# Kernel tuning notes

Hardware: AMD Instinct MI355X
Metric: run time of the kernel (lower is better)

The kernel has to match this reference:

```python
import jax, jax.numpy as jnp
import numpy as np

B, C, H, W = 64, 256, 56, 56
SCALES = (1, 2, 4, 8)  # scale[:groups] with groups=4; sum = 15 pooled maps


def setup_inputs() -> dict:
    key = jax.random.key(0)
    k1, k2 = jax.random.split(key)
    x = jax.random.normal(k1, (B, C, H, W), dtype=jnp.float32)
    # weight: [num_fea=H*W, sum(scales)=15]; small init (original fills 0, which
    # would make the gate identically sigmoid(0)=0.5 — use small random instead)
    weight = jax.random.normal(k2, (H * W, 15), dtype=jnp.float32) * 0.02
    return {"x": x, "weight": weight}


def reference(x, weight):
    b, c, h, w = x.shape
    hw = h * w
    # Multi-scale channel-group mean pooling: for scale i, split channels into
    # i equal groups (c divisible by all scales) and mean over each group.
    # Equivalent to the original's loop of c*j//i : c*(j+1)//i slices.
    feats = [x.reshape(b, i, c // i, hw).mean(axis=2) for i in SCALES]
    t = jnp.concatenate(feats, axis=1)  # [b, 15, hw]
    # Points(): normalize across the 15 pooled features per spatial location
    mean = t.mean(axis=1, keepdims=True)           # [b, 1, hw]
    std = t.std(axis=1, keepdims=True)             # unbiased=False (ddof=0)
    tn = (t - mean) / std                          # [b, 15, hw]
    # _style_integration: per-pixel weighted sum over the 15 features
    z = jnp.einsum('bfs,sf->bs', tn, weight)       # [b, hw]
    gate = jax.nn.sigmoid(z).reshape(b, 1, h, w)
    return x * gate
```

## Files before the change

kernel.cpp:

```cpp
#include <hip/hip_runtime.h>
#include <math.h>


constexpr int C_   = 256;
constexpr int HW_  = 3136;
constexpr int B_   = 64;
constexpr int SPW_ = 16;
constexpr int TPI_ = HW_ / SPW_;
constexpr int WPB_ = 4;

__device__ __forceinline__ float4 shx4(float4 a, int m) {
  float4 r;
  r.x = __shfl_xor(a.x, m);
  r.y = __shfl_xor(a.y, m);
  r.z = __shfl_xor(a.z, m);
  r.w = __shfl_xor(a.w, m);
  return r;
}
__device__ __forceinline__ float4 add4(float4 a, float4 b) {
  float4 r; r.x = a.x + b.x; r.y = a.y + b.y; r.z = a.z + b.z; r.w = a.w + b.w;
  return r;
}

__global__ __launch_bounds__(256, 4) void ppca_fused(
    const float* __restrict__ x, const float* __restrict__ wgt,
    float* __restrict__ out)
{
  const int lane = threadIdx.x & 63;
  const int wav  = threadIdx.x >> 6;
  const unsigned W   = blockIdx.x * WPB_ + wav;
  const unsigned b   = W / TPI_;
  const unsigned til = W - b * TPI_;
  const int sp0 = til * SPW_;

  const int s4 = lane & 3;
  const int c0 = lane >> 2;

  const size_t off = (size_t)b * C_ * HW_ + (size_t)c0 * 16 * HW_
                   + (size_t)sp0 + (size_t)(s4 << 2);
  const float* xb = x + off;
  float* ob = out + off;

  float4 v[16];
  #pragma unroll
  for (int i = 0; i < 16; ++i)
    v[i] = *(const float4*)(xb + (size_t)i * HW_);

  float4 ps = v[0];
  #pragma unroll
  for (int i = 1; i < 16; ++i) ps = add4(ps, v[i]);

  const float4 t1 = add4(ps, shx4(ps, 4));
  const float4 t2 = add4(t1, shx4(t1, 8));
  const float4 t3 = add4(t2, shx4(t2, 16));
  const float4 t4 = add4(t3, shx4(t3, 32));

  float4 m4;
  m4.x = t4.x * (1.f / 256.f); m4.y = t4.y * (1.f / 256.f);
  m4.z = t4.z * (1.f / 256.f); m4.w = t4.w * (1.f / 256.f);

  const float* wr = wgt + (size_t)sp0 * 15;
  const int i128 = 1 + (c0 >> 3);
  const int i64  = 3 + (c0 >> 2);
  const int i32  = 7 + (c0 >> 1);

  float4 zn, sq;
#define DO_SPATIAL(J, T1c, T2c, T3c, Mc, ZNc, SQc)                           \
  {                                                                          \
    const float* wp = wr + ((s4 << 2) + J) * 15;                             \
    const float w128 = wp[i128];                                             \
    const float w64  = wp[i64];                                              \
    const float w32  = wp[i32];                                              \
    const float u1 = T1c * (1.f / 32.f)  - Mc;                               \
    const float u2 = T2c * (1.f / 64.f)  - Mc;                               \
    const float u3 = T3c * (1.f / 128.f) - Mc;                               \
    ZNc = u1 * w32 * 0.5f + u2 * w64 * 0.25f + u3 * w128 * 0.125f;           \
    SQc = u1 * u1 * 0.5f  + u2 * u2 * 0.25f  + u3 * u3 * 0.125f;             \
  }
  DO_SPATIAL(0, t1.x, t2.x, t3.x, m4.x, zn.x, sq.x)
  DO_SPATIAL(1, t1.y, t2.y, t3.y, m4.y, zn.y, sq.y)
  DO_SPATIAL(2, t1.z, t2.z, t3.z, m4.z, zn.z, sq.z)
  DO_SPATIAL(3, t1.w, t2.w, t3.w, m4.w, zn.w, sq.w)
#undef DO_SPATIAL

  #pragma unroll
  for (int d = 4; d <= 32; d <<= 1) {
    zn = add4(zn, shx4(zn, d));
    sq = add4(sq, shx4(sq, d));
  }

  float4 g;
#define GATE(ZNc, SQc, Gc)                                                   \
  {                                                                          \
    const float var = SQc * (1.f / 15.f);                                    \
    const float inv = 1.f / sqrtf(var);                                      \
    const float z   = ZNc * inv;                                             \
    Gc = 1.f / (1.f + __expf(-z));                                           \
  }
  GATE(zn.x, sq.x, g.x)
  GATE(zn.y, sq.y, g.y)
  GATE(zn.z, sq.z, g.z)
  GATE(zn.w, sq.w, g.w)
#undef GATE

  #pragma unroll
  for (int i = 0; i < 16; ++i) {
    float4 vv = v[i];
    vv.x *= g.x; vv.y *= g.y; vv.z *= g.z; vv.w *= g.w;
    *(float4*)(ob + (size_t)i * HW_) = vv;
  }
}

extern "C" void kernel_launch(void* const* d_in, const int* in_sizes, int n_in,
                              void* d_out, int out_size, void* d_ws, size_t ws_size,
                              hipStream_t stream) {
  const float* x = (const float*)d_in[0];
  const float* w = (const float*)d_in[1];
  float* out = (float*)d_out;
  (void)in_sizes; (void)n_in; (void)out_size; (void)d_ws; (void)ws_size;

  dim3 grid(B_ * TPI_ / WPB_);
  dim3 block(256);
  ppca_fused<<<grid, block, 0, stream>>>(x, w, out);
}
```

Before: 343.0 us.

## Process multiple spatial tiles per wave with double-buffered register prefetch

Each wave now handles 8 consecutive tiles of 8 spatial positions instead of one tile of 16. The next tile's loads are issued into a second register buffer before the current tile is reduced and stored, so memory latency overlaps with compute. Lane mapping changes to 32 channel groups by 2 spatial quads, with one more shuffle reduction stage. The grid shrinks by a factor of K, and two 8-element float4 buffers raise register pressure, which may limit occupancy.

```diff
diff --git a/kernel.cpp b/kernel.cpp
--- a/kernel.cpp
+++ b/kernel.cpp
@@ -5,9 +5,12 @@
 constexpr int C_   = 256;
 constexpr int HW_  = 3136;
 constexpr int B_   = 64;
-constexpr int SPW_ = 16;
+constexpr int SPW_ = 8;
 constexpr int TPI_ = HW_ / SPW_;
+constexpr int NT_  = B_ * TPI_;
+constexpr int K_   = 8;
 constexpr int WPB_ = 4;
+constexpr int GRID_ = NT_ / (K_ * WPB_);
 
 __device__ __forceinline__ float4 shx4(float4 a, int m) {
   float4 r;
@@ -22,60 +25,59 @@
   return r;
 }
 
-__global__ __launch_bounds__(256, 4) void ppca_fused(
-    const float* __restrict__ x, const float* __restrict__ wgt,
-    float* __restrict__ out)
-{
-  const int lane = threadIdx.x & 63;
-  const int wav  = threadIdx.x >> 6;
-  const unsigned W   = blockIdx.x * WPB_ + wav;
-  const unsigned b   = W / TPI_;
-  const unsigned til = W - b * TPI_;
-  const int sp0 = til * SPW_;
+__device__ __forceinline__ const float* tbase(const float* x, unsigned t,
+                                              int c0, int s4) {
+  const unsigned b   = t / TPI_;
+  const unsigned til = t - b * TPI_;
+  return x + (size_t)b * C_ * HW_ + (size_t)c0 * 8 * HW_
+           + (size_t)(til * SPW_) + (size_t)(s4 << 2);
+}
 
-  const int s4 = lane & 3;
-  const int c0 = lane >> 2;
+__device__ __forceinline__ void tload(float4 v[8], const float* x, unsigned t,
+                                      int c0, int s4) {
+  const float* p = tbase(x, t, c0, s4);
+  #pragma unroll
+  for (int i = 0; i < 8; ++i)
+    v[i] = *(const float4*)(p + (size_t)i * HW_);
+}
 
-  const size_t off = (size_t)b * C_ * HW_ + (size_t)c0 * 16 * HW_
-                   + (size_t)sp0 + (size_t)(s4 << 2);
-  const float* xb = x + off;
-  float* ob = out + off;
-
-  float4 v[16];
-  #pragma unroll
-  for (int i = 0; i < 16; ++i)
-    v[i] = *(const float4*)(xb + (size_t)i * HW_);
-
+__device__ __forceinline__ void tcs(float4 v[8], const float* __restrict__ x,
+                                    const float* __restrict__ wgt,
+                                    float* __restrict__ out, unsigned t,
+                                    int c0, int s4) {
   float4 ps = v[0];
   #pragma unroll
-  for (int i = 1; i < 16; ++i) ps = add4(ps, v[i]);
-
-  const float4 t1 = add4(ps, shx4(ps, 4));
-  const float4 t2 = add4(t1, shx4(t1, 8));
-  const float4 t3 = add4(t2, shx4(t2, 16));
-  const float4 t4 = add4(t3, shx4(t3, 32));
+  for (int i = 1; i < 8; ++i) ps = add4(ps, v[i]);
+  const float4 p16 = add4(ps,  shx4(ps, 2));
+  const float4 t1  = add4(p16, shx4(p16, 4));
+  const float4 t2  = add4(t1,  shx4(t1, 8));
+  const float4 t3  = add4(t2,  shx4(t2, 16));
+  const float4 t4  = add4(t3,  shx4(t3, 32));
 
   float4 m4;
   m4.x = t4.x * (1.f / 256.f); m4.y = t4.y * (1.f / 256.f);
   m4.z = t4.z * (1.f / 256.f); m4.w = t4.w * (1.f / 256.f);
 
-  const float* wr = wgt + (size_t)sp0 * 15;
-  const int i128 = 1 + (c0 >> 3);
-  const int i64  = 3 + (c0 >> 2);
-  const int i32  = 7 + (c0 >> 1);
+  const unsigned b   = t / TPI_;
+  const unsigned til = t - b * TPI_;
+  const int sp0 = (int)(til * SPW_);
+  const float* wr = wgt + (size_t)(sp0 + (s4 << 2)) * 15;
+  const int i128 = 1 + (c0 >> 4);
+  const int i64  = 3 + (c0 >> 3);
+  const int i32  = 7 + (c0 >> 2);
 
   float4 zn, sq;
 #define DO_SPATIAL(J, T1c, T2c, T3c, Mc, ZNc, SQc)                           \
   {                                                                          \
-    const float* wp = wr + ((s4 << 2) + J) * 15;                             \
+    const float* wp = wr + (J) * 15;                                         \
     const float w128 = wp[i128];                                             \
     const float w64  = wp[i64];                                              \
     const float w32  = wp[i32];                                              \
     const float u1 = T1c * (1.f / 32.f)  - Mc;                               \
     const float u2 = T2c * (1.f / 64.f)  - Mc;                               \
     const float u3 = T3c * (1.f / 128.f) - Mc;                               \
-    ZNc = u1 * w32 * 0.5f + u2 * w64 * 0.25f + u3 * w128 * 0.125f;           \
-    SQc = u1 * u1 * 0.5f  + u2 * u2 * 0.25f  + u3 * u3 * 0.125f;             \
+    ZNc = u1 * w32 * 0.25f + u2 * w64 * 0.125f + u3 * w128 * 0.0625f;        \
+    SQc = u1 * u1 * 0.25f  + u2 * u2 * 0.125f  + u3 * u3 * 0.0625f;          \
   }
   DO_SPATIAL(0, t1.x, t2.x, t3.x, m4.x, zn.x, sq.x)
   DO_SPATIAL(1, t1.y, t2.y, t3.y, m4.y, zn.y, sq.y)
@@ -84,7 +86,7 @@
 #undef DO_SPATIAL
 
   #pragma unroll
-  for (int d = 4; d <= 32; d <<= 1) {
+  for (int d = 2; d <= 32; d <<= 1) {
     zn = add4(zn, shx4(zn, d));
     sq = add4(sq, shx4(sq, d));
   }
@@ -92,10 +94,8 @@
   float4 g;
 #define GATE(ZNc, SQc, Gc)                                                   \
   {                                                                          \
-    const float var = SQc * (1.f / 15.f);                                    \
-    const float inv = 1.f / sqrtf(var);                                      \
-    const float z   = ZNc * inv;                                             \
-    Gc = 1.f / (1.f + __expf(-z));                                           \
+    const float inv = 1.f / sqrtf(SQc * (1.f / 15.f));                       \
+    Gc = 1.f / (1.f + __expf(-(ZNc * inv)));                                 \
   }
   GATE(zn.x, sq.x, g.x)
   GATE(zn.y, sq.y, g.y)
@@ -103,12 +103,39 @@
   GATE(zn.w, sq.w, g.w)
 #undef GATE
 
+  float* ob = (float*)tbase(out, t, c0, s4);
   #pragma unroll
-  for (int i = 0; i < 16; ++i) {
+  for (int i = 0; i < 8; ++i) {
     float4 vv = v[i];
     vv.x *= g.x; vv.y *= g.y; vv.z *= g.z; vv.w *= g.w;
     *(float4*)(ob + (size_t)i * HW_) = vv;
   }
+}
+
+__global__ __launch_bounds__(256, 4) void ppca_fused(
+    const float* __restrict__ x, const float* __restrict__ wgt,
+    float* __restrict__ out)
+{
+  const int lane = threadIdx.x & 63;
+  const int wav  = threadIdx.x >> 6;
+  const int s4 = lane & 1;
+  const int c0 = lane >> 1;
+
+  const unsigned w  = blockIdx.x * WPB_ + wav;
+  const unsigned t0 = w * K_;
+
+  float4 A[8], Bv[8];
+  tload(A,  x, t0 + 0, c0, s4);
+  tload(Bv, x, t0 + 1, c0, s4);
+
+  tcs(A,  x, wgt, out, t0 + 0, c0, s4); tload(A,  x, t0 + 2, c0, s4);
+  tcs(Bv, x, wgt, out, t0 + 1, c0, s4); tload(Bv, x, t0 + 3, c0, s4);
+  tcs(A,  x, wgt, out, t0 + 2, c0, s4); tload(A,  x, t0 + 4, c0, s4);
+  tcs(Bv, x, wgt, out, t0 + 3, c0, s4); tload(Bv, x, t0 + 5, c0, s4);
+  tcs(A,  x, wgt, out, t0 + 4, c0, s4); tload(A,  x, t0 + 6, c0, s4);
+  tcs(Bv, x, wgt, out, t0 + 5, c0, s4); tload(Bv, x, t0 + 7, c0, s4);
+  tcs(A,  x, wgt, out, t0 + 6, c0, s4);
+  tcs(Bv, x, wgt, out, t0 + 7, c0, s4);
 }
 
 extern "C" void kernel_launch(void* const* d_in, const int* in_sizes, int n_in,
@@ -119,7 +146,7 @@
   float* out = (float*)d_out;
   (void)in_sizes; (void)n_in; (void)out_size; (void)d_ws; (void)ws_size;
 
-  dim3 grid(B_ * TPI_ / WPB_);
+  dim3 grid(GRID_);
   dim3 block(256);
   ppca_fused<<<grid, block, 0, stream>>>(x, w, out);
 }
```

Measured after the change: 515.0 us. 1.5x slower.
